# Optimization experiments

Hardware: AMD Instinct MI355X
Metric: run time of the kernel (lower is better)

## Reference

```python
import jax, jax.numpy as jnp
import numpy as np


def setup_inputs() -> dict:
    key = jax.random.key(0)
    k1, k2 = jax.random.split(key)
    N_rays, N_samples, NJ = 4096, 96, 24
    pts = jax.random.normal(k1, (N_rays, N_samples, 3), dtype=jnp.float32)
    skts = jax.random.normal(k2, (N_rays, NJ, 4, 4), dtype=jnp.float32)
    return {"pts": pts, "skts": skts}


def reference(pts, skts):
    # pts: [R, S, 3] -> homogeneous [R, S, 4]
    pts_h = jnp.concatenate([pts, jnp.ones(pts.shape[:-1] + (1,), dtype=pts.dtype)], axis=-1)
    # skts: [R, J, 4, 4]; fused equivalent of expand/transpose/matmul/permute:
    # out[r, s, j, a] = sum_b skts[r, j, a, b] * pts_h[r, s, b]
    out = jnp.einsum("rjab,rsb->rsja", skts, pts_h)
    return out[..., :3]
```

## Files before the change

kernel.cpp:

```cpp
#include <hip/hip_runtime.h>


constexpr int S_DIM = 96;
constexpr int J_DIM = 24;
constexpr int SKT_STRIDE = 17;
constexpr int BLOCK = 256;
constexpr int PAIRS = S_DIM * J_DIM;
constexpr int ITERS = PAIRS / BLOCK;

__global__ __launch_bounds__(BLOCK) void w2l_kernel(
    const float* __restrict__ pts,
    const float* __restrict__ skts,
    float* __restrict__ out) {

    const int r = blockIdx.x;
    const int tid = threadIdx.x;

    __shared__ float s_skt[J_DIM * SKT_STRIDE];
    __shared__ float s_pts[S_DIM * 3];

    const float* __restrict__ skt_g = skts + (size_t)r * (J_DIM * 16);
    const float* __restrict__ pts_g = pts  + (size_t)r * (S_DIM * 3);

    for (int i = tid; i < J_DIM * 16 + S_DIM * 3; i += BLOCK) {
        if (i < J_DIM * 16) {
            s_skt[(i >> 4) * SKT_STRIDE + (i & 15)] = skt_g[i];
        } else {
            int k = i - J_DIM * 16;
            s_pts[k] = pts_g[k];
        }
    }
    __syncthreads();

    float* __restrict__ out_r = out + (size_t)r * (PAIRS * 3);

    #pragma unroll
    for (int it = 0; it < ITERS; ++it) {
        const int p = tid + it * BLOCK;
        const int s = p / J_DIM;
        const int j = p - s * J_DIM;

        const float x = s_pts[s * 3 + 0];
        const float y = s_pts[s * 3 + 1];
        const float z = s_pts[s * 3 + 2];

        const float* __restrict__ b = &s_skt[j * SKT_STRIDE];
        const float o0 = fmaf(b[0], x, fmaf(b[1], y, fmaf(b[2],  z, b[3])));
        const float o1 = fmaf(b[4], x, fmaf(b[5], y, fmaf(b[6],  z, b[7])));
        const float o2 = fmaf(b[8], x, fmaf(b[9], y, fmaf(b[10], z, b[11])));

        *reinterpret_cast<float3*>(out_r + (size_t)p * 3) = make_float3(o0, o1, o2);
    }
}

extern "C" void kernel_launch(void* const* d_in, const int* in_sizes, int n_in,
                              void* d_out, int out_size, void* d_ws, size_t ws_size,
                              hipStream_t stream) {
    const float* pts  = (const float*)d_in[0];
    const float* skts = (const float*)d_in[1];
    float* out = (float*)d_out;

    const int R = in_sizes[0] / (S_DIM * 3);
    w2l_kernel<<<R, BLOCK, 0, stream>>>(pts, skts, out);
}
```

Baseline: 25.14 us.

## Hoist per-joint transform into registers and use nontemporal vector stores

Raises the block to 384 threads so each thread keeps a fixed joint index across iterations. Its three transform rows are loaded into registers once instead of being re-read from LDS for every sample. Points are stored padded to float4 with w=1 and the skinning matrices are loaded with float4 global loads. Outputs use nontemporal stores to cut cache pollution on the large write stream. Because the kernel is dominated by output bandwidth, the benefit may be limited, and the larger block could affect occupancy.

```diff
diff --git a/kernel.cpp b/kernel.cpp
--- a/kernel.cpp
+++ b/kernel.cpp
@@ -3,53 +3,60 @@
 
 constexpr int S_DIM = 96;
 constexpr int J_DIM = 24;
-constexpr int SKT_STRIDE = 17;
-constexpr int BLOCK = 256;
-constexpr int PAIRS = S_DIM * J_DIM;
-constexpr int ITERS = PAIRS / BLOCK;
+constexpr int BLOCK = 384;
+constexpr int SKT_STR   = 20;
+constexpr int SKT_WORDS = J_DIM * SKT_STR;
+constexpr int PTS_WORDS = S_DIM * 4;
+constexpr int ITERS = S_DIM * J_DIM / BLOCK;
+constexpr int RAY_FLOATS = S_DIM * J_DIM * 3;
+
+typedef float f32x3 __attribute__((ext_vector_type(3)));
 
 __global__ __launch_bounds__(BLOCK) void w2l_kernel(
     const float* __restrict__ pts,
     const float* __restrict__ skts,
     float* __restrict__ out) {
 
-    const int r = blockIdx.x;
     const int tid = threadIdx.x;
+    const int r   = blockIdx.x;
 
-    __shared__ float s_skt[J_DIM * SKT_STRIDE];
-    __shared__ float s_pts[S_DIM * 3];
+    __shared__ __align__(16) float s_skt[SKT_WORDS];
+    __shared__ __align__(16) float s_pts[PTS_WORDS];
 
-    const float* __restrict__ skt_g = skts + (size_t)r * (J_DIM * 16);
-    const float* __restrict__ pts_g = pts  + (size_t)r * (S_DIM * 3);
-
-    for (int i = tid; i < J_DIM * 16 + S_DIM * 3; i += BLOCK) {
-        if (i < J_DIM * 16) {
-            s_skt[(i >> 4) * SKT_STRIDE + (i & 15)] = skt_g[i];
-        } else {
-            int k = i - J_DIM * 16;
-            s_pts[k] = pts_g[k];
-        }
+    if (tid < 96) {
+        float4 v = reinterpret_cast<const float4*>(skts + (size_t)r * (J_DIM * 16))[tid];
+        int jj = tid >> 2, a = tid & 3;
+        *reinterpret_cast<float4*>(&s_skt[jj * SKT_STR + a * 4]) = v;
+        s_pts[tid * 4 + 3] = 1.0f;
+    } else {
+        int q = tid - 96;
+        float v = pts[(size_t)r * (S_DIM * 3) + q];
+        int s = q / 3, c = q - 3 * s;
+        s_pts[s * 4 + c] = v;
     }
     __syncthreads();
 
-    float* __restrict__ out_r = out + (size_t)r * (PAIRS * 3);
+    const int s0 = tid / J_DIM;
+    const int j  = tid - s0 * J_DIM;
+
+    const float4 B0 = *reinterpret_cast<const float4*>(&s_skt[j * SKT_STR + 0]);
+    const float4 B1 = *reinterpret_cast<const float4*>(&s_skt[j * SKT_STR + 4]);
+    const float4 B2 = *reinterpret_cast<const float4*>(&s_skt[j * SKT_STR + 8]);
+
+    float* __restrict__ out_r = out + (size_t)r * RAY_FLOATS;
 
     #pragma unroll
     for (int it = 0; it < ITERS; ++it) {
+        const int s = s0 + it * 16;
+        const float4 P = *reinterpret_cast<const float4*>(&s_pts[s * 4]);
+
+        f32x3 o;
+        o.x = fmaf(B0.x, P.x, fmaf(B0.y, P.y, fmaf(B0.z, P.z, B0.w)));
+        o.y = fmaf(B1.x, P.x, fmaf(B1.y, P.y, fmaf(B1.z, P.z, B1.w)));
+        o.z = fmaf(B2.x, P.x, fmaf(B2.y, P.y, fmaf(B2.z, P.z, B2.w)));
+
         const int p = tid + it * BLOCK;
-        const int s = p / J_DIM;
-        const int j = p - s * J_DIM;
-
-        const float x = s_pts[s * 3 + 0];
-        const float y = s_pts[s * 3 + 1];
-        const float z = s_pts[s * 3 + 2];
-
-        const float* __restrict__ b = &s_skt[j * SKT_STRIDE];
-        const float o0 = fmaf(b[0], x, fmaf(b[1], y, fmaf(b[2],  z, b[3])));
-        const float o1 = fmaf(b[4], x, fmaf(b[5], y, fmaf(b[6],  z, b[7])));
-        const float o2 = fmaf(b[8], x, fmaf(b[9], y, fmaf(b[10], z, b[11])));
-
-        *reinterpret_cast<float3*>(out_r + (size_t)p * 3) = make_float3(o0, o1, o2);
+        __builtin_nontemporal_store(o, reinterpret_cast<f32x3*>(out_r + (size_t)p * 3));
     }
 }
 
```

Result: no change. 24.84 us (-1.2%).
